# Performance work log

Measured on AMD Instinct MI355X. Metric: run time of the kernel, lower is better.

The kernel has to match this reference:

```python
import jax, jax.numpy as jnp
import numpy as np

PH, PW, SR = 7, 7, 2  # aligned_height, aligned_width, sampling_ratio


def setup_inputs() -> dict:
    key = jax.random.key(0)
    k1, k2, k3, k4 = jax.random.split(key, 4)
    B, C, H, W, N = 2, 256, 200, 200, 1000
    features = jax.random.normal(k1, (B, C, H, W), dtype=jnp.float32)
    # build valid boxes [x1, y1, x2, y2] in feature-map pixel coords
    ctr = jax.random.uniform(k2, (N, 2), minval=0.0, maxval=float(W))
    half = jax.random.uniform(k3, (N, 2), minval=2.0, maxval=50.0)
    xy1 = jnp.clip(ctr - half, 0.0, float(W) - 1.0)
    xy2 = jnp.clip(ctr + half, 0.0, float(W) - 1.0)
    rois = jnp.concatenate([xy1, xy2], axis=1).astype(jnp.float32)  # [N,4]
    sample_indices = jax.random.randint(k4, (N,), 0, B).astype(jnp.int32)
    return {"features": features, "rois": rois, "sample_indices": sample_indices}


def _roi_align(features, rois, sample_indices):
    B, C, H, W = features.shape
    N = rois.shape[0]
    feats = jnp.transpose(features, (0, 2, 3, 1))  # [B,H,W,C] for gather locality
    x1, y1, x2, y2 = rois[:, 0], rois[:, 1], rois[:, 2], rois[:, 3]
    roi_w = jnp.maximum(x2 - x1, 1.0)
    roi_h = jnp.maximum(y2 - y1, 1.0)
    bin_h = roi_h / PH
    bin_w = roi_w / PW
    g = SR
    # sample point t in [0, PH*g): y = y1 + (t + 0.5)/g * bin_h (Detectron grid)
    ty = (jnp.arange(PH * g, dtype=jnp.float32) + 0.5) / g  # [PH*g]
    tx = (jnp.arange(PW * g, dtype=jnp.float32) + 0.5) / g  # [PW*g]
    ys = y1[:, None] + ty[None, :] * bin_h[:, None]  # [N, PH*g]
    xs = x1[:, None] + tx[None, :] * bin_w[:, None]  # [N, PW*g]
    valid_y = (ys >= -1.0) & (ys <= H)
    valid_x = (xs >= -1.0) & (xs <= W)
    yc = jnp.clip(ys, 0.0, H - 1.0)
    xc = jnp.clip(xs, 0.0, W - 1.0)
    y0 = jnp.floor(yc).astype(jnp.int32)
    x0 = jnp.floor(xc).astype(jnp.int32)
    y1i = jnp.minimum(y0 + 1, H - 1)
    x1i = jnp.minimum(x0 + 1, W - 1)
    ly = yc - y0.astype(jnp.float32)  # [N, PH*g]
    lx = xc - x0.astype(jnp.float32)  # [N, PW*g]
    hy, hx = 1.0 - ly, 1.0 - lx
    b = sample_indices.astype(jnp.int32)[:, None, None]  # [N,1,1]
    Y0, Y1 = y0[:, :, None], y1i[:, :, None]              # [N,Th,1]
    X0, X1 = x0[:, None, :], x1i[:, None, :]              # [N,1,Tw]
    # bilinear weights, zeroed outside the valid range (kernel semantics)
    mask = (valid_y[:, :, None] & valid_x[:, None, :]).astype(feats.dtype)
    w00 = (hy[:, :, None] * hx[:, None, :] * mask)[..., None]
    w01 = (hy[:, :, None] * lx[:, None, :] * mask)[..., None]
    w10 = (ly[:, :, None] * hx[:, None, :] * mask)[..., None]
    w11 = (ly[:, :, None] * lx[:, None, :] * mask)[..., None]
    vals = (w00 * feats[b, Y0, X0]
            + w01 * feats[b, Y0, X1]
            + w10 * feats[b, Y1, X0]
            + w11 * feats[b, Y1, X1])  # [N, PH*g, PW*g, C]
    out = vals.reshape(N, PH, g, PW, g, C).mean(axis=(2, 4))  # avg over samples
    return jnp.transpose(out, (0, 3, 1, 2))  # [N, C, PH, PW]


def reference(features, rois, sample_indices):
    return _roi_align(features, rois, sample_indices)
```

## Files before the change

### kernel.cpp

```cpp
#include <hip/hip_runtime.h>

#define CCH 256
#define HH 200
#define WW 200
#define HWW (HH * WW)
#define PHB 7
#define PWB 7
#define NBINS 49
#define OUTSZ (CCH * NBINS)

typedef float f4v __attribute__((ext_vector_type(4)));
typedef unsigned short us4 __attribute__((ext_vector_type(4)));
typedef unsigned u2v __attribute__((ext_vector_type(2)));
typedef unsigned u4v __attribute__((ext_vector_type(4)));

__device__ __forceinline__ unsigned short f2bf(float f) {
  unsigned u = __builtin_bit_cast(unsigned, f);
  u += 0x7fffu + ((u >> 16) & 1u);
  return (unsigned short)(u >> 16);
}
__device__ __forceinline__ float bf_lo(unsigned u) {
  return __builtin_bit_cast(float, u << 16);
}
__device__ __forceinline__ float bf_hi(unsigned u) {
  return __builtin_bit_cast(float, u & 0xffff0000u);
}

__global__ __launch_bounds__(256) void transpose_kernel(
    const float* __restrict__ in, unsigned short* __restrict__ out) {
  __shared__ float tile[64][65];
  const int b  = blockIdx.z;
  const int p0 = blockIdx.x * 64;
  const int c0 = blockIdx.y * 64;
  const int t  = threadIdx.x;
  const int k  = t & 15;
  const int r0 = t >> 4;
  const float* ip = in  + (size_t)b * CCH * HWW;
  unsigned short* op = out + (size_t)b * HWW * CCH;
#pragma unroll
  for (int rr = 0; rr < 4; ++rr) {
    const int c = r0 + rr * 16;
    const f4v v = __builtin_nontemporal_load(
        (const f4v*)(ip + (size_t)(c0 + c) * HWW + p0 + 4 * k));
    tile[c][4 * k + 0] = v.x;
    tile[c][4 * k + 1] = v.y;
    tile[c][4 * k + 2] = v.z;
    tile[c][4 * k + 3] = v.w;
  }
  __syncthreads();
#pragma unroll
  for (int rr = 0; rr < 4; ++rr) {
    const int p = r0 + rr * 16;
    us4 v;
    v.x = f2bf(tile[4 * k + 0][p]);
    v.y = f2bf(tile[4 * k + 1][p]);
    v.z = f2bf(tile[4 * k + 2][p]);
    v.w = f2bf(tile[4 * k + 3][p]);
    *(us4*)(op + (size_t)(p0 + p) * CCH + c0 + 4 * k) = v;
  }
}

struct __align__(16) Tap {
  unsigned off[4];
  float    w[4];
};

__global__ __launch_bounds__(256) void roi_kernel(
    const unsigned short* __restrict__ feat, const float* __restrict__ rois,
    const int* __restrict__ sidx, float* __restrict__ out) {
  __shared__ float s_out[64 * NBINS];
  __shared__ Tap   s_tab[196];

  const int n  = blockIdx.x >> 2;
  const int hq = blockIdx.x & 3;
  const int t  = threadIdx.x;
  const int bb = sidx[n];

  if (t < 196) {
    const float x1 = rois[n * 4 + 0];
    const float y1 = rois[n * 4 + 1];
    const float x2 = rois[n * 4 + 2];
    const float y2 = rois[n * 4 + 3];
    const float bin_w = fmaxf(x2 - x1, 1.0f) * (1.0f / 7.0f);
    const float bin_h = fmaxf(y2 - y1, 1.0f) * (1.0f / 7.0f);
    const int iy = t / 14;
    const int ix = t - iy * 14;
    const float ys = y1 + ((float)iy + 0.5f) * 0.5f * bin_h;
    const float xs = x1 + ((float)ix + 0.5f) * 0.5f * bin_w;
    const float vy = (ys >= -1.0f && ys <= (float)HH) ? 1.0f : 0.0f;
    const float vx = (xs >= -1.0f && xs <= (float)WW) ? 1.0f : 0.0f;
    const float yc = fminf(fmaxf(ys, 0.0f), (float)(HH - 1));
    const float xc = fminf(fmaxf(xs, 0.0f), (float)(WW - 1));
    const int yy0 = (int)yc;
    const int xx0 = (int)xc;
    const int yy1 = min(yy0 + 1, HH - 1);
    const int xx1 = min(xx0 + 1, WW - 1);
    const float ly = yc - (float)yy0, hy = 1.0f - ly;
    const float lx = xc - (float)xx0, hx = 1.0f - lx;
    const float f = vy * vx * 0.25f;
    const unsigned r0 = (unsigned)(yy0 * WW);
    const unsigned r1 = (unsigned)(yy1 * WW);
    s_tab[t].off[0] = (r0 + (unsigned)xx0) * (CCH * 2);
    s_tab[t].off[1] = (r0 + (unsigned)xx1) * (CCH * 2);
    s_tab[t].off[2] = (r1 + (unsigned)xx0) * (CCH * 2);
    s_tab[t].off[3] = (r1 + (unsigned)xx1) * (CCH * 2);
    s_tab[t].w[0] = f * hy * hx;
    s_tab[t].w[1] = f * hy * lx;
    s_tab[t].w[2] = f * ly * hx;
    s_tab[t].w[3] = f * ly * lx;
  }
  __syncthreads();

  const int lane = t & 63;
  const int wv   = t >> 6;
  const int lq   = lane >> 4;
  const unsigned laneoff = (unsigned)((lane & 15) << 3);
  const char* __restrict__ base =
      (const char*)feat + ((size_t)bb * HWW * CCH + 64 * hq) * 2;

#pragma unroll 1
  for (int p = wv; p < 13; p += 4) {
    const int mybin = 4 * p + lq;
    const int bin   = min(mybin, NBINS - 1);
    const int ph  = bin / PWB;
    const int pw  = bin - ph * PWB;
    const int s00 = (2 * ph) * 14 + 2 * pw;
    float a0 = 0.0f, a1 = 0.0f, a2 = 0.0f, a3 = 0.0f;
#pragma unroll
    for (int sy = 0; sy < 2; ++sy) {
#pragma unroll
      for (int sx = 0; sx < 2; ++sx) {
        const Tap* tp = &s_tab[s00 + sy * 14 + sx];
        const u4v o4 = *(const u4v*)tp->off;
        const f4v w4 = *(const f4v*)tp->w;
        const u2v q00 = *(const u2v*)(base + (o4.x + laneoff));
        const u2v q01 = *(const u2v*)(base + (o4.y + laneoff));
        const u2v q10 = *(const u2v*)(base + (o4.z + laneoff));
        const u2v q11 = *(const u2v*)(base + (o4.w + laneoff));
        a0 += w4.x * bf_lo(q00.x) + w4.y * bf_lo(q01.x)
            + w4.z * bf_lo(q10.x) + w4.w * bf_lo(q11.x);
        a1 += w4.x * bf_hi(q00.x) + w4.y * bf_hi(q01.x)
            + w4.z * bf_hi(q10.x) + w4.w * bf_hi(q11.x);
        a2 += w4.x * bf_lo(q00.y) + w4.y * bf_lo(q01.y)
            + w4.z * bf_lo(q10.y) + w4.w * bf_lo(q11.y);
        a3 += w4.x * bf_hi(q00.y) + w4.y * bf_hi(q01.y)
            + w4.z * bf_hi(q10.y) + w4.w * bf_hi(q11.y);
      }
    }
    if (mybin < NBINS) {
      const int c0 = (lane & 15) << 2;
      s_out[(c0 + 0) * NBINS + mybin] = a0;
      s_out[(c0 + 1) * NBINS + mybin] = a1;
      s_out[(c0 + 2) * NBINS + mybin] = a2;
      s_out[(c0 + 3) * NBINS + mybin] = a3;
    }
  }
  __syncthreads();

  const f4v* so4 = (const f4v*)s_out;
  f4v*       on4 = (f4v*)(out + (size_t)n * OUTSZ + hq * (64 * NBINS));
  for (int i = t; i < (64 * NBINS) / 4; i += 256) on4[i] = so4[i];
}

__global__ __launch_bounds__(256) void roi_kernel_nchw(
    const float* __restrict__ feat, const float* __restrict__ rois,
    const int* __restrict__ sidx, float* __restrict__ out) {
  __shared__ float s_out[OUTSZ];
  __shared__ int   s_yi[2][14];
  __shared__ int   s_xi[2][14];
  __shared__ float s_ly[14], s_hy[14], s_vy[14];
  __shared__ float s_lx[14], s_hx[14], s_vx[14];
  const int n = blockIdx.x;
  const int t = threadIdx.x;
  const float x1 = rois[n * 4 + 0], y1 = rois[n * 4 + 1];
  const float x2 = rois[n * 4 + 2], y2 = rois[n * 4 + 3];
  const int   bb = sidx[n];
  const float bin_w = fmaxf(x2 - x1, 1.0f) / 7.0f;
  const float bin_h = fmaxf(y2 - y1, 1.0f) / 7.0f;
  if (t < 14) {
    const float tt = ((float)t + 0.5f) * 0.5f;
    const float ys = y1 + tt * bin_h;
    s_vy[t] = (ys >= -1.0f && ys <= (float)HH) ? 1.0f : 0.0f;
    const float yc = fminf(fmaxf(ys, 0.0f), (float)(HH - 1));
    const int yy0 = (int)yc, yy1 = min(yy0 + 1, HH - 1);
    s_yi[0][t] = yy0 * WW; s_yi[1][t] = yy1 * WW;
    s_ly[t] = yc - (float)yy0; s_hy[t] = 1.0f - s_ly[t];
  } else if (t < 28) {
    const int i = t - 14;
    const float tt = ((float)i + 0.5f) * 0.5f;
    const float xs = x1 + tt * bin_w;
    s_vx[i] = (xs >= -1.0f && xs <= (float)WW) ? 1.0f : 0.0f;
    const float xc = fminf(fmaxf(xs, 0.0f), (float)(WW - 1));
    const int xx0 = (int)xc, xx1 = min(xx0 + 1, WW - 1);
    s_xi[0][i] = xx0; s_xi[1][i] = xx1;
    s_lx[i] = xc - (float)xx0; s_hx[i] = 1.0f - s_lx[i];
  }
  __syncthreads();
  const int c = t;
  const float* Fb = feat + ((size_t)bb * CCH + c) * HWW;
  for (int bin = 0; bin < NBINS; ++bin) {
    const int ph = bin / PWB, pw = bin - ph * PWB;
    float acc = 0.0f;
    for (int sy = 0; sy < 2; ++sy) {
      const int iy = ph * 2 + sy;
      for (int sx = 0; sx < 2; ++sx) {
        const int ix = pw * 2 + sx;
        const float m = s_vy[iy] * s_vx[ix];
        acc += m * (s_hy[iy] * (s_hx[ix] * Fb[s_yi[0][iy] + s_xi[0][ix]] +
                                s_lx[ix] * Fb[s_yi[0][iy] + s_xi[1][ix]]) +
                    s_ly[iy] * (s_hx[ix] * Fb[s_yi[1][iy] + s_xi[0][ix]] +
                                s_lx[ix] * Fb[s_yi[1][iy] + s_xi[1][ix]]));
      }
    }
    s_out[c * NBINS + bin] = acc * 0.25f;
  }
  __syncthreads();
  float* on = out + (size_t)n * OUTSZ;
  for (int i = t; i < OUTSZ; i += 256) on[i] = s_out[i];
}

extern "C" void kernel_launch(void* const* d_in, const int* in_sizes, int n_in,
                              void* d_out, int out_size, void* d_ws, size_t ws_size,
                              hipStream_t stream) {
  const float* features = (const float*)d_in[0];
  const float* rois     = (const float*)d_in[1];
  const int*   sidx     = (const int*)d_in[2];
  float*       out      = (float*)d_out;

  const int N = in_sizes[1] / 4;
  const int B = in_sizes[0] / (CCH * HWW);

  const size_t need = (size_t)B * HWW * CCH * sizeof(unsigned short);
  if (ws_size >= need) {
    unsigned short* ft = (unsigned short*)d_ws;
    dim3 tgrid(HWW / 64, CCH / 64, B);
    transpose_kernel<<<tgrid, 256, 0, stream>>>(features, ft);
    roi_kernel<<<4 * N, 256, 0, stream>>>(ft, rois, sidx, out);
  } else {
    roi_kernel_nchw<<<N, 256, 0, stream>>>(features, rois, sidx, out);
  }
}
```

Before: 171.7 us.

## Sort ROIs by Morton order and remap workgroups per XCD for L2 locality

Adds a single-block bitonic sort that orders ROIs by batch index and a Morton code of their centers. The roi kernel then remaps block IDs so that consecutive sorted ROIs land on the same XCD. The goal is to raise L2 hit rates for gathers from overlapping feature regions. The cost is an extra serial kernel launch and one more level of indirection through the permutation.

```diff
diff --git a/kernel.cpp b/kernel.cpp
--- a/kernel.cpp
+++ b/kernel.cpp
@@ -60,6 +60,49 @@
   }
 }
 
+__global__ __launch_bounds__(1024) void sort_kernel(
+    const float* __restrict__ rois, const int* __restrict__ sidx,
+    const int n, int* __restrict__ perm) {
+  const int t = threadIdx.x;
+  if (n > 1024) {
+    for (int i = t; i < n; i += 1024) perm[i] = i;
+    return;
+  }
+  __shared__ unsigned s_key[1024];
+  __shared__ int      s_idx[1024];
+  unsigned key = 0xFFFFFFFFu;
+  if (t < n) {
+    const float cx = 0.5f * (rois[4 * t + 0] + rois[4 * t + 2]);
+    const float cy = 0.5f * (rois[4 * t + 1] + rois[4 * t + 3]);
+    int qx = (int)(cx * 0.125f); qx = qx < 0 ? 0 : (qx > 31 ? 31 : qx);
+    int qy = (int)(cy * 0.125f); qy = qy < 0 ? 0 : (qy > 31 ? 31 : qy);
+    unsigned m = 0;
+#pragma unroll
+    for (int i = 0; i < 5; ++i)
+      m |= (((unsigned)(qy >> i) & 1u) << (2 * i + 1)) |
+           (((unsigned)(qx >> i) & 1u) << (2 * i));
+    key = ((unsigned)sidx[t] << 10) | m;
+  }
+  s_key[t] = key;
+  s_idx[t] = t;
+  __syncthreads();
+  for (int k = 2; k <= 1024; k <<= 1) {
+    for (int j = k >> 1; j > 0; j >>= 1) {
+      const int p = t ^ j;
+      if (p > t) {
+        const unsigned a = s_key[t], b = s_key[p];
+        const bool up = ((t & k) == 0);
+        if (up ? (a > b) : (a < b)) {
+          s_key[t] = b; s_key[p] = a;
+          const int ti = s_idx[t]; s_idx[t] = s_idx[p]; s_idx[p] = ti;
+        }
+      }
+      __syncthreads();
+    }
+  }
+  if (t < n) perm[t] = s_idx[t];
+}
+
 struct __align__(16) Tap {
   unsigned off[4];
   float    w[4];
@@ -67,12 +110,20 @@
 
 __global__ __launch_bounds__(256) void roi_kernel(
     const unsigned short* __restrict__ feat, const float* __restrict__ rois,
-    const int* __restrict__ sidx, float* __restrict__ out) {
+    const int* __restrict__ sidx, const int* __restrict__ perm,
+    float* __restrict__ out) {
   __shared__ float s_out[64 * NBINS];
   __shared__ Tap   s_tab[196];
 
-  const int n  = blockIdx.x >> 2;
-  const int hq = blockIdx.x & 3;
+  const unsigned nwg  = gridDim.x;
+  const unsigned orig = blockIdx.x;
+  const unsigned q8   = nwg >> 3, r8 = nwg & 7;
+  const unsigned xcd  = orig & 7, ii = orig >> 3;
+  const unsigned j    =
+      (xcd < r8 ? xcd * (q8 + 1) : r8 * (q8 + 1) + (xcd - r8) * q8) + ii;
+
+  const int n  = perm[j >> 2];
+  const int hq = j & 3;
   const int t  = threadIdx.x;
   const int bb = sidx[n];
 
@@ -230,12 +281,15 @@
   const int N = in_sizes[1] / 4;
   const int B = in_sizes[0] / (CCH * HWW);
 
-  const size_t need = (size_t)B * HWW * CCH * sizeof(unsigned short);
+  const size_t slab = (size_t)B * HWW * CCH * sizeof(unsigned short);
+  const size_t need = slab + (size_t)N * sizeof(int);
   if (ws_size >= need) {
-    unsigned short* ft = (unsigned short*)d_ws;
+    unsigned short* ft   = (unsigned short*)d_ws;
+    int*            perm = (int*)((char*)d_ws + slab);
+    sort_kernel<<<1, 1024, 0, stream>>>(rois, sidx, N, perm);
     dim3 tgrid(HWW / 64, CCH / 64, B);
     transpose_kernel<<<tgrid, 256, 0, stream>>>(features, ft);
-    roi_kernel<<<4 * N, 256, 0, stream>>>(ft, rois, sidx, out);
+    roi_kernel<<<4 * N, 256, 0, stream>>>(ft, rois, sidx, perm, out);
   } else {
     roi_kernel_nchw<<<N, 256, 0, stream>>>(features, rois, sidx, out);
   }
```

Measured after the change: 179.6 us. 4.6% more time.
